# Optimization experiments

Hardware: AMD Instinct MI355X
Metric: run time of the kernel (lower is better)

## Reference

```python
import jax, jax.numpy as jnp
import numpy as np

B = 512
IMG = 32
NFF = 64
LAT_N = 256
LAT_C = 100
TOKEN_DIM = 3 + 2 * NFF  # 131
HEADS = 4
DEPTH = 2
MLP_HID = 4 * LAT_C
EPS = 1e-5


def _layernorm(x, g, b):
    mu = jnp.mean(x, axis=-1, keepdims=True)
    var = jnp.mean((x - mu) ** 2, axis=-1, keepdims=True)
    return (x - mu) * jax.lax.rsqrt(var + EPS) * g + b


def _mha(h, in_w, in_b, out_w, out_b):
    # torch nn.MultiheadAttention, batch_first, eval mode (no dropout)
    Bh, L, D = h.shape
    hd = D // HEADS
    qkv = h @ in_w.T + in_b  # [B, L, 3D]
    q, k, v = jnp.split(qkv, 3, axis=-1)
    def heads(t):
        return t.reshape(Bh, L, HEADS, hd).transpose(0, 2, 1, 3)  # [B,H,L,hd]
    q, k, v = heads(q), heads(k), heads(v)
    scores = jnp.einsum('bhqd,bhkd->bhqk', q, k) / jnp.sqrt(jnp.float32(hd))
    attn = jax.nn.softmax(scores, axis=-1)
    o = jnp.einsum('bhqk,bhkd->bhqd', attn, v)
    o = o.transpose(0, 2, 1, 3).reshape(Bh, L, D)
    return o @ out_w.T + out_b


def _forward(x, latents, latent_pos, fourier_matrix, proj_w, proj_b,
             q_w, q_b, k_w, k_b, v_w, v_b, o_w, o_b,
             ln1_g, ln1_b, attn_in_w, attn_in_b, attn_out_w, attn_out_b,
             ln2_g, ln2_b, mlp_w1, mlp_b1, mlp_w2, mlp_b2):
    Bx = x.shape[0]
    lat = (latents + latent_pos)[None].repeat(Bx, axis=0)  # [B, 256, 100]

    # per-pixel RGB tokens
    rgb = x.transpose(0, 2, 3, 1).reshape(Bx, -1, 3)  # [B, 1024, 3]

    # Fourier positional encoding
    yy, xx = jnp.meshgrid(jnp.arange(IMG, dtype=jnp.float32),
                          jnp.arange(IMG, dtype=jnp.float32), indexing='ij')
    coords = jnp.stack([xx / (IMG - 1), yy / (IMG - 1)], axis=-1).reshape(-1, 2)  # [1024, 2]
    proj = coords @ fourier_matrix  # [1024, NFF]
    pos = jnp.concatenate([jnp.cos(2 * jnp.pi * proj), jnp.sin(2 * jnp.pi * proj)], axis=-1)
    pos = jnp.broadcast_to(pos[None], (Bx, IMG * IMG, 2 * NFF))

    tokens = jnp.concatenate([rgb, pos], axis=-1)  # [B, 1024, 131]
    tokens = tokens @ proj_w.T + proj_b  # [B, 1024, 100]

    # K/V depend only on (fixed) tokens, identical across the 8 iterations
    k = tokens @ k_w.T + k_b
    v = tokens @ v_w.T + v_b

    scale = 1.0 / jnp.sqrt(jnp.float32(LAT_C))
    for _ in range(8):
        q = lat @ q_w.T + q_b  # [B, 256, 100]
        attn = jax.nn.softmax(jnp.einsum('bqc,bkc->bqk', q, k) * scale, axis=-1)
        lat = jnp.einsum('bqk,bkc->bqc', attn, v) @ o_w.T + o_b
        # latent transformer (depth=2, shared across the 8 iterations)
        for d in range(DEPTH):
            h = _layernorm(lat, ln1_g[d], ln1_b[d])
            lat = lat + _mha(h, attn_in_w[d], attn_in_b[d], attn_out_w[d], attn_out_b[d])
            h = _layernorm(lat, ln2_g[d], ln2_b[d])
            h = jax.nn.gelu(h @ mlp_w1[d].T + mlp_b1[d], approximate=False) @ mlp_w2[d].T + mlp_b2[d]
            lat = lat + h
    return lat.mean(axis=1)  # [B, 100]


def setup_inputs() -> dict:
    key = jax.random.key(0)
    ks = jax.random.split(key, 32)
    s = 0.02
    inp = {
        'x': jax.random.normal(ks[0], (B, 3, IMG, IMG), jnp.float32),
        'latents': jax.random.normal(ks[1], (LAT_N, LAT_C), jnp.float32),
        'latent_pos': jax.random.normal(ks[2], (LAT_N, LAT_C), jnp.float32),
        'fourier_matrix': jax.random.normal(ks[3], (2, NFF), jnp.float32),
        'proj_w': jax.random.normal(ks[4], (LAT_C, TOKEN_DIM), jnp.float32) * s,
        'proj_b': jnp.zeros((LAT_C,), jnp.float32),
        'q_w': jax.random.normal(ks[5], (LAT_C, LAT_C), jnp.float32) * s,
        'q_b': jnp.zeros((LAT_C,), jnp.float32),
        'k_w': jax.random.normal(ks[6], (LAT_C, LAT_C), jnp.float32) * s,
        'k_b': jnp.zeros((LAT_C,), jnp.float32),
        'v_w': jax.random.normal(ks[7], (LAT_C, LAT_C), jnp.float32) * s,
        'v_b': jnp.zeros((LAT_C,), jnp.float32),
        'o_w': jax.random.normal(ks[8], (LAT_C, LAT_C), jnp.float32) * s,
        'o_b': jnp.zeros((LAT_C,), jnp.float32),
        'ln1_g': jnp.ones((DEPTH, LAT_C), jnp.float32),
        'ln1_b': jnp.zeros((DEPTH, LAT_C), jnp.float32),
        'attn_in_w': jax.random.normal(ks[9], (DEPTH, 3 * LAT_C, LAT_C), jnp.float32) * s,
        'attn_in_b': jnp.zeros((DEPTH, 3 * LAT_C), jnp.float32),
        'attn_out_w': jax.random.normal(ks[10], (DEPTH, LAT_C, LAT_C), jnp.float32) * s,
        'attn_out_b': jnp.zeros((DEPTH, LAT_C), jnp.float32),
        'ln2_g': jnp.ones((DEPTH, LAT_C), jnp.float32),
        'ln2_b': jnp.zeros((DEPTH, LAT_C), jnp.float32),
        'mlp_w1': jax.random.normal(ks[11], (DEPTH, MLP_HID, LAT_C), jnp.float32) * s,
        'mlp_b1': jnp.zeros((DEPTH, MLP_HID), jnp.float32),
        'mlp_w2': jax.random.normal(ks[12], (DEPTH, LAT_C, MLP_HID), jnp.float32) * s,
        'mlp_b2': jnp.zeros((DEPTH, LAT_C), jnp.float32),
    }
    return inp


def reference(x, latents, latent_pos, fourier_matrix, proj_w, proj_b,
              q_w, q_b, k_w, k_b, v_w, v_b, o_w, o_b,
              ln1_g, ln1_b, attn_in_w, attn_in_b, attn_out_w, attn_out_b,
              ln2_g, ln2_b, mlp_w1, mlp_b1, mlp_w2, mlp_b2):
    return _forward(x, latents, latent_pos, fourier_matrix, proj_w, proj_b,
                    q_w, q_b, k_w, k_b, v_w, v_b, o_w, o_b,
                    ln1_g, ln1_b, attn_in_w, attn_in_b, attn_out_w, attn_out_b,
                    ln2_g, ln2_b, mlp_w1, mlp_b1, mlp_w2, mlp_b2)
```

## Files before the change

### kernel.cpp

```cpp
#include <hip/hip_runtime.h>
#include <cmath>

#define WS_AK 0
#define WS_AV 300
#define WS_U  600

#define UW_DK   0
#define UW_DV   106496
#define UW_QW   212992
#define UW_OW   227328
#define UW_W1   241664
#define UW_W2   344064
#define UW_AIW  444416
#define UW_AOW  542720
#define UW_WCNT 358400

typedef __attribute__((ext_vector_type(8))) short short8;
typedef __attribute__((ext_vector_type(4))) float f32x4;

#define MFMA(a, b, c) __builtin_amdgcn_mfma_f32_16x16x32_bf16((a), (b), (c), 0, 0, 0)

static __device__ __forceinline__ unsigned short f2bf(float f) {
  unsigned int u = __float_as_uint(f);
  u += 0x7FFF + ((u >> 16) & 1);
  return (unsigned short)(u >> 16);
}
static __device__ __forceinline__ float bf2f(unsigned short u) {
  return __uint_as_float(((unsigned int)u) << 16);
}
static __device__ __forceinline__ f32x4 zero4() { return (f32x4){0.f, 0.f, 0.f, 0.f}; }

__global__ void pre_amat_kernel(const float* __restrict__ proj_w,
                                const float* __restrict__ k_w,
                                const float* __restrict__ v_w,
                                float* __restrict__ ws) {
  int idx = blockIdx.x * blockDim.x + threadIdx.x;
  if (idx >= 600) return;
  int sel = idx / 300;
  int rem = idx % 300;
  int c = rem / 100, m = rem % 100;
  const float* w = sel ? v_w : k_w;
  float acc = 0.f;
  for (int n = 0; n < 100; ++n) acc += proj_w[n * 131 + c] * w[m * 100 + n];
  ws[(sel ? WS_AV : WS_AK) + c * 100 + m] = acc;
}

__global__ void pre_dmat_kernel(const float* __restrict__ fm,
                                const float* __restrict__ proj_w,
                                const float* __restrict__ proj_b,
                                const float* __restrict__ k_w,
                                const float* __restrict__ k_b,
                                const float* __restrict__ v_w,
                                const float* __restrict__ v_b,
                                unsigned short* __restrict__ uw) {
  __shared__ float pos[8][128];
  __shared__ float tc[8][100];
  int p0 = blockIdx.x * 8;
  int tid = threadIdx.x;
  for (int idx = tid; idx < 1024; idx += 256) {
    int pl = idx >> 7, f = idx & 127;
    int p = p0 + pl;
    float cx = (float)(p & 31) * (1.f / 31.f);
    float cy = (float)(p >> 5) * (1.f / 31.f);
    int fi = f & 63;
    float pr = cx * fm[fi] + cy * fm[64 + fi];
    float ang = 6.2831853071795864769f * pr;
    pos[pl][f] = (f < 64) ? cosf(ang) : sinf(ang);
  }
  __syncthreads();
  for (int idx = tid; idx < 800; idx += 256) {
    int pl = idx / 100, n = idx % 100;
    float acc = proj_b[n];
    const float* pw = proj_w + n * 131 + 3;
    for (int f = 0; f < 128; ++f) acc += pos[pl][f] * pw[f];
    tc[pl][n] = acc;
  }
  __syncthreads();
  for (int idx = tid; idx < 1600; idx += 256) {
    int sel = idx / 800;
    int rem = idx % 800;
    int pl = rem / 100, m = rem % 100;
    const float* w = sel ? v_w : k_w;
    float acc = sel ? v_b[m] : k_b[m];
    for (int n = 0; n < 100; ++n) acc += tc[pl][n] * w[m * 100 + n];
    if (sel) uw[UW_DV + m * 1024 + (p0 + pl)] = f2bf(acc);
    else     uw[UW_DK + (p0 + pl) * 104 + m] = f2bf(acc);
  }
  for (int idx = tid; idx < 32; idx += 256) {
    int pl = idx >> 2, mm = 100 + (idx & 3);
    uw[UW_DK + (p0 + pl) * 104 + mm] = 0;
  }
}

__global__ void pre_wfrag_kernel(const float* __restrict__ q_w,
                                 const float* __restrict__ o_w,
                                 const float* __restrict__ mlp_w1,
                                 const float* __restrict__ mlp_w2,
                                 const float* __restrict__ attn_in_w,
                                 const float* __restrict__ attn_out_w,
                                 unsigned short* __restrict__ uw) {
  int idx = blockIdx.x * 256 + threadIdx.x;
  if (idx >= UW_WCNT) return;
  float val = 0.f;
  if (idx < 14336) {
    int rem = idx;
    int kt = rem / 3584; rem %= 3584;
    int nt = rem / 512;  rem %= 512;
    int lane = rem >> 3, j = rem & 7;
    int k = kt * 32 + (lane >> 4) * 8 + j;
    int n = nt * 16 + (lane & 15);
    if (k < 100 && n < 100) val = q_w[n * 100 + k];
  } else if (idx < 28672) {
    int rem = idx - 14336;
    int kt = rem / 3584; rem %= 3584;
    int nt = rem / 512;  rem %= 512;
    int lane = rem >> 3, j = rem & 7;
    int k = kt * 32 + (lane >> 4) * 8 + j;
    int n = nt * 16 + (lane & 15);
    if (k < 100 && n < 100) val = o_w[n * 100 + k];
  } else if (idx < 131072) {
    int off = idx - 28672;
    int dd = off / 51200;
    int rem = off % 51200;
    int kt = rem / 12800; rem %= 12800;
    int nt = rem / 512;   rem %= 512;
    int lane = rem >> 3, j = rem & 7;
    int k = kt * 32 + (lane >> 4) * 8 + j;
    int n = nt * 16 + (lane & 15);
    if (k < 100) val = mlp_w1[dd * 40000 + n * 100 + k];
  } else if (idx < 231424) {
    int off = idx - 131072;
    int dd = off / 50176;
    int rem = off % 50176;
    int kt = rem / 3584; rem %= 3584;
    int nt = rem / 512;  rem %= 512;
    int lane = rem >> 3, j = rem & 7;
    int k = kt * 32 + (lane >> 4) * 8 + j;
    int n = nt * 16 + (lane & 15);
    if (k < 400 && n < 100) val = mlp_w2[dd * 40000 + n * 400 + k];
  } else if (idx < 329728) {
    int off = idx - 231424;
    int dw = off / 16384;
    int rem = off % 16384;
    int dd = dw / 3, wsel = dw % 3;
    int kt = rem / 4096; rem %= 4096;
    int nt = rem / 512;  rem %= 512;
    int lane = rem >> 3, j = rem & 7;
    int k = kt * 32 + (lane >> 4) * 8 + j;
    int np = nt * 16 + (lane & 15);
    int hh = np >> 5, dh = np & 31;
    if (k < 100 && dh < 25)
      val = attn_in_w[dd * 30000 + (wsel * 100 + hh * 25 + dh) * 100 + k];
  } else {
    int off = idx - 329728;
    int dd = off / 14336;
    int rem = off % 14336;
    int kt = rem / 3584; rem %= 3584;
    int nt = rem / 512;  rem %= 512;
    int lane = rem >> 3, j = rem & 7;
    int kp = kt * 32 + (lane >> 4) * 8 + j;
    int hh = kp >> 5, dh = kp & 31;
    int n = nt * 16 + (lane & 15);
    if (dh < 25 && n < 100)
      val = attn_out_w[dd * 10000 + n * 100 + hh * 25 + dh];
  }
  uw[UW_QW + idx] = f2bf(val);
}

__launch_bounds__(512, 1)
__global__ void perceiver_kernel(
    const float* __restrict__ x,
    const float* __restrict__ latents,
    const float* __restrict__ latent_pos,
    const float* __restrict__ q_b, const float* __restrict__ o_b,
    const float* __restrict__ ln1_g, const float* __restrict__ ln1_b,
    const float* __restrict__ attn_in_b, const float* __restrict__ attn_out_b,
    const float* __restrict__ ln2_g, const float* __restrict__ ln2_b,
    const float* __restrict__ mlp_b1, const float* __restrict__ mlp_b2,
    const float* __restrict__ ws,
    float* __restrict__ out) {
  __shared__ __align__(16) float s_pool[39240];
  float* s_sm = s_pool;
  float* reg0 = s_pool + 3400;
  unsigned short* s_M  = (unsigned short*)reg0;
  unsigned short* s_Hb = (unsigned short*)(reg0 + 17408);
  unsigned short* sK = s_Hb;
  unsigned short* sV = s_Hb + 8192;
  unsigned short* sP = s_Hb + 15360;
  unsigned short* s_Qh  = s_Hb;
  unsigned short* kfrag = s_Hb + 10240;
  unsigned short* vfrag = s_Hb + 18432;
  unsigned short* sPm   = s_Hb + 26624;
  float* s_x = reg0;

  const int tid  = threadIdx.x;
  const int b    = blockIdx.x;
  const int r    = tid >> 1;
  const int half = tid & 1;
  const int hc   = half * 50;
  const int lane = tid & 63;
  const int wv   = tid >> 6;
  const int li   = lane & 15;
  const int lg   = lane >> 4;
  const unsigned short* uw = (const unsigned short*)(ws + WS_U);

  for (int i = tid; i < 100; i += 512) { s_sm[i] = q_b[i]; s_sm[100 + i] = o_b[i]; }
  for (int i = tid; i < 200; i += 512) {
    s_sm[200 + i] = ln1_g[i]; s_sm[400 + i] = ln1_b[i];
    s_sm[600 + i] = ln2_g[i]; s_sm[800 + i] = ln2_b[i];
    s_sm[1600 + i] = attn_out_b[i]; s_sm[2600 + i] = mlp_b2[i];
  }
  for (int i = tid; i < 600; i += 512) s_sm[1000 + i] = attn_in_b[i];
  for (int i = tid; i < 800; i += 512) s_sm[1800 + i] = mlp_b1[i];
  for (int i = tid; i < 300; i += 512) { s_sm[2800 + i] = ws[WS_AK + i]; s_sm[3100 + i] = ws[WS_AV + i]; }

  float latv[50];
  #pragma unroll
  for (int i = 0; i < 50; ++i)
    latv[i] = latents[r * 100 + hc + i] + latent_pos[r * 100 + hc + i];

  const float* xb = x + (long)b * 3072;

  for (int it = 0; it < 8; ++it) {
    __syncthreads();
    #pragma unroll
    for (int i = 0; i < 50; ++i) s_M[r * 136 + hc + i] = f2bf(latv[i]);
    #pragma unroll
    for (int i = 0; i < 14; ++i) s_M[r * 136 + 100 + half * 14 + i] = 0;
    __syncthreads();

    {
      f32x4 qacc[2][7];
      #pragma unroll
      for (int a0 = 0; a0 < 2; ++a0)
        #pragma unroll
        for (int a1 = 0; a1 < 7; ++a1) qacc[a0][a1] = zero4();
      short8 aq[2][4];
      #pragma unroll
      for (int mt2 = 0; mt2 < 2; ++mt2)
        #pragma unroll
        for (int kt = 0; kt < 4; ++kt)
          aq[mt2][kt] = *(const short8*)(s_M + ((2 * wv + mt2) * 16 + li) * 136 + kt * 32 + lg * 8);
      #pragma unroll
      for (int nt = 0; nt < 7; ++nt)
        #pragma unroll
        for (int kt = 0; kt < 4; ++kt) {
          short8 bw = *(const short8*)(uw + UW_QW + ((kt * 7 + nt) * 64 + lane) * 8);
          #pragma unroll
          for (int mt2 = 0; mt2 < 2; ++mt2) qacc[mt2][nt] = MFMA(aq[mt2][kt], bw, qacc[mt2][nt]);
        }
      #pragma unroll
      for (int mt2 = 0; mt2 < 2; ++mt2)
        #pragma unroll
        for (int nt = 0; nt < 7; ++nt) {
          int col = nt * 16 + li;
          if (col < 100) {
            #pragma unroll
            for (int rg = 0; rg < 4; ++rg) {
              int row = (2 * wv + mt2) * 16 + lg * 4 + rg;
              s_M[row * 136 + col] = f2bf((qacc[mt2][nt][rg] + s_sm[col]) * 0.1f);
            }
          }
        }
    }

    f32x4 O[2][7];
    #pragma unroll
    for (int a0 = 0; a0 < 2; ++a0)
      #pragma unroll
      for (int a1 = 0; a1 < 7; ++a1) O[a0][a1] = zero4();
    short8 aq2[2][4];
    #pragma unroll
    for (int mt2 = 0; mt2 < 2; ++mt2)
      #pragma unroll
      for (int kt = 0; kt < 4; ++kt)
        aq2[mt2][kt] = *(const short8*)(s_M + ((2 * wv + mt2) * 16 + li) * 136 + kt * 32 + lg * 8);

    for (int t0 = 0; t0 < 1024; t0 += 64) {
      __syncthreads();
      for (int vi = tid; vi < 1024; vi += 512) {
        const int key = vi & 63, cg = vi >> 6;
        const int p = t0 + key;
        short8 w;
        if (cg < 13) {
          const float xr = xb[p], xg = xb[1024 + p], xv = xb[2048 + p];
          short8 dk = *(const short8*)(uw + UW_DK + p * 104 + cg * 8);
          #pragma unroll
          for (int e = 0; e < 8; ++e) {
            const int c = cg * 8 + e;
            float val = 0.f;
            if (c < 100)
              val = xr * s_sm[2800 + c] + xg * s_sm[2900 + c] + xv * s_sm[3000 + c]
                  + bf2f((unsigned short)w[0] * 0 + (unsigned short)dk[e]);
            w[e] = (short)f2bf(val);
          }
        } else {
          #pragma unroll
          for (int e = 0; e < 8; ++e) w[e] = 0;
        }
        *(short8*)(sK + vi * 8) = w;
      }
      for (int vi = tid; vi < 896; vi += 512) {
        const int ch = vi % 112, kg = vi / 112;
        const int pv0 = t0 + kg * 8;
        short8 w;
        if (ch < 100) {
          const float4 xr0 = *(const float4*)(xb + pv0);
          const float4 xr1 = *(const float4*)(xb + pv0 + 4);
          const float4 xg0 = *(const float4*)(xb + 1024 + pv0);
          const float4 xg1 = *(const float4*)(xb + 1024 + pv0 + 4);
          const float4 xv0 = *(const float4*)(xb + 2048 + pv0);
          const float4 xv1 = *(const float4*)(xb + 2048 + pv0 + 4);
          short8 dv = *(const short8*)(uw + UW_DV + ch * 1024 + pv0);
          const float a0 = s_sm[3100 + ch], a1 = s_sm[3200 + ch], a2 = s_sm[3300 + ch];
          const float xrv[8] = {xr0.x, xr0.y, xr0.z, xr0.w, xr1.x, xr1.y, xr1.z, xr1.w};
          const float xgv[8] = {xg0.x, xg0.y, xg0.z, xg0.w, xg1.x, xg1.y, xg1.z, xg1.w};
          const float xvv[8] = {xv0.x, xv0.y, xv0.z, xv0.w, xv1.x, xv1.y, xv1.z, xv1.w};
          #pragma unroll
          for (int e = 0; e < 8; ++e)
            w[e] = (short)f2bf(xrv[e] * a0 + xgv[e] * a1 + xvv[e] * a2
                               + bf2f((unsigned short)dv[e]));
        } else if (ch == 100) {
          #pragma unroll
          for (int e = 0; e < 8; ++e) w[e] = (short)0x3F80;
        } else {
          #pragma unroll
          for (int e = 0; e < 8; ++e) w[e] = 0;
        }
        *(short8*)(sV + vi * 8) = w;
      }
      __syncthreads();

      #pragma unroll
      for (int ntk = 0; ntk < 4; ++ntk) {
        short8 bk[4];
        #pragma unroll
        for (int kt = 0; kt < 4; ++kt)
          bk[kt] = *(const short8*)(sK + ((kt * 4 + lg) * 64 + ntk * 16 + li) * 8);
        #pragma unroll
        for (int mt2 = 0; mt2 < 2; ++mt2) {
          f32x4 sres = zero4();
          #pragma unroll
          for (int kt = 0; kt < 4; ++kt) sres = MFMA(aq2[mt2][kt], bk[kt], sres);
          #pragma unroll
          for (int rg = 0; rg < 4; ++rg) {
            int row = (2 * wv + mt2) * 16 + lg * 4 + rg;
            sP[row * 72 + ntk * 16 + li] = f2bf(__expf(sres[rg]));
          }
        }
      }
      short8 ap[2][2];
      #pragma unroll
      for (int mt2 = 0; mt2 < 2; ++mt2)
        #pragma unroll
        for (int kt2 = 0; kt2 < 2; ++kt2)
          ap[mt2][kt2] = *(const short8*)(sP + ((2 * wv + mt2) * 16 + li) * 72 + kt2 * 32 + lg * 8);
      #pragma unroll
      for (int nt = 0; nt < 7; ++nt) {
        short8 bv0 = *(const short8*)(sV + ((0 + lg) * 112 + nt * 16 + li) * 8);
        short8 bv1 = *(const short8*)(sV + ((4 + lg) * 112 + nt * 16 + li) * 8);
        #pragma unroll
        for (int mt2 = 0; mt2 < 2; ++mt2) {
          O[mt2][nt] = MFMA(ap[mt2][0], bv0, O[mt2][nt]);
          O[mt2][nt] = MFMA(ap[mt2][1], bv1, O[mt2][nt]);
        }
      }
    }

    {
      #pragma unroll
      for (int mt2 = 0; mt2 < 2; ++mt2) {
        float linv[4];
        #pragma unroll
        for (int rg = 0; rg < 4; ++rg) {
          float lv = __shfl(O[mt2][6][rg], (lane & 48) + 4);
          linv[rg] = 1.0f / lv;
        }
        #pragma unroll
        for (int nt = 0; nt < 7; ++nt) {
          int col = nt * 16 + li;
          if (col < 100) {
            #pragma unroll
            for (int rg = 0; rg < 4; ++rg) {
              int row = (2 * wv + mt2) * 16 + lg * 4 + rg;
              s_M[row * 136 + col] = f2bf(O[mt2][nt][rg] * linv[rg]);
            }
          }
        }
      }
    }

    {
      f32x4 lacc[2][7];
      #pragma unroll
      for (int a0 = 0; a0 < 2; ++a0)
        #pragma unroll
        for (int a1 = 0; a1 < 7; ++a1) lacc[a0][a1] = zero4();
      short8 ao[2][4];
      #pragma unroll
      for (int mt2 = 0; mt2 < 2; ++mt2)
        #pragma unroll
        for (int kt = 0; kt < 4; ++kt)
          ao[mt2][kt] = *(const short8*)(s_M + ((2 * wv + mt2) * 16 + li) * 136 + kt * 32 + lg * 8);
      #pragma unroll
      for (int nt = 0; nt < 7; ++nt)
        #pragma unroll
        for (int kt = 0; kt < 4; ++kt) {
          short8 bw = *(const short8*)(uw + UW_OW + ((kt * 7 + nt) * 64 + lane) * 8);
          #pragma unroll
          for (int mt2 = 0; mt2 < 2; ++mt2) lacc[mt2][nt] = MFMA(ao[mt2][kt], bw, lacc[mt2][nt]);
        }
      __syncthreads();
      #pragma unroll
      for (int mt2 = 0; mt2 < 2; ++mt2)
        #pragma unroll
        for (int nt = 0; nt < 7; ++nt) {
          int col = nt * 16 + li;
          if (col < 100) {
            #pragma unroll
            for (int rg = 0; rg < 4; ++rg) {
              int row = (2 * wv + mt2) * 16 + lg * 4 + rg;
              s_x[row * 104 + col] = lacc[mt2][nt][rg] + s_sm[100 + col];
            }
          }
        }
      __syncthreads();
      #pragma unroll
      for (int i = 0; i < 50; ++i) latv[i] = s_x[r * 104 + hc + i];
      __syncthreads();
    }

    for (int d = 0; d < 2; ++d) {
      float hv[50];
      {
        float s = 0.f, sq = 0.f;
        #pragma unroll
        for (int i = 0; i < 50; ++i) { s += latv[i]; sq += latv[i] * latv[i]; }
        s += __shfl_xor(s, 1); sq += __shfl_xor(sq, 1);
        float mu = s * 0.01f;
        float var = sq * 0.01f - mu * mu;
        float rs = rsqrtf(var + 1e-5f);
        #pragma unroll
        for (int i = 0; i < 50; ++i)
          hv[i] = (latv[i] - mu) * rs * s_sm[200 + d * 100 + hc + i] + s_sm[400 + d * 100 + hc + i];
      }

      #pragma unroll
      for (int i = 0; i < 50; ++i) s_M[r * 136 + hc + i] = f2bf(hv[i]);
      #pragma unroll
      for (int i = 0; i < 14; ++i) s_M[r * 136 + 100 + half * 14 + i] = 0;
      short8 ah[2][4];
      #pragma unroll
      for (int mt2 = 0; mt2 < 2; ++mt2)
        #pragma unroll
        for (int kt = 0; kt < 4; ++kt)
          ah[mt2][kt] = *(const short8*)(s_M + ((2 * wv + mt2) * 16 + li) * 136 + kt * 32 + lg * 8);

      for (int h = 0; h < 4; ++h) {
        __syncthreads();
        f32x4 cq[2][2], ck[2][2], cv[2][2];
        #pragma unroll
        for (int a0 = 0; a0 < 2; ++a0)
          #pragma unroll
          for (int a1 = 0; a1 < 2; ++a1) { cq[a0][a1] = zero4(); ck[a0][a1] = zero4(); cv[a0][a1] = zero4(); }
        #pragma unroll
        for (int ntd = 0; ntd < 2; ++ntd)
          #pragma unroll
          for (int kt = 0; kt < 4; ++kt) {
            const int bidx = ((kt * 8 + h * 2 + ntd) * 64 + lane) * 8;
            short8 bq  = *(const short8*)(uw + UW_AIW + (d * 3 + 0) * 16384 + bidx);
            short8 bkk = *(const short8*)(uw + UW_AIW + (d * 3 + 1) * 16384 + bidx);
            short8 bvv = *(const short8*)(uw + UW_AIW + (d * 3 + 2) * 16384 + bidx);
            #pragma unroll
            for (int mt2 = 0; mt2 < 2; ++mt2) {
              cq[mt2][ntd] = MFMA(ah[mt2][kt], bq,  cq[mt2][ntd]);
              ck[mt2][ntd] = MFMA(ah[mt2][kt], bkk, ck[mt2][ntd]);
              cv[mt2][ntd] = MFMA(ah[mt2][kt], bvv, cv[mt2][ntd]);
            }
          }
        #pragma unroll
        for (int mt2 = 0; mt2 < 2; ++mt2)
          #pragma unroll
          for (int ntd = 0; ntd < 2; ++ntd) {
            const int dh = ntd * 16 + li;
            const bool ok = dh < 25;
            const float qb2 = ok ? s_sm[1000 + d * 300 +       h * 25 + dh] : 0.f;
            const float kb2 = ok ? s_sm[1000 + d * 300 + 100 + h * 25 + dh] : 0.f;
            const float vb2 = ok ? s_sm[1000 + d * 300 + 200 + h * 25 + dh] : 0.f;
            #pragma unroll
            for (int rg = 0; rg < 4; ++rg) {
              const int rr = lg * 4 + rg;
              const int row = (2 * wv + mt2) * 16 + rr;
              s_Qh[row * 40 + dh] = ok ? f2bf((cq[mt2][ntd][rg] + qb2) * 0.2f) : 0;
              kfrag[((2 * wv + mt2) * 64 + (dh >> 3) * 16 + rr) * 8 + (dh & 7)] =
                  ok ? f2bf(ck[mt2][ntd][rg] + kb2) : 0;
              vfrag[((wv * 2 + ntd) * 64 + (mt2 * 2 + (rr >> 3)) * 16 + li) * 8 + (rr & 7)] =
                  ok ? f2bf(cv[mt2][ntd][rg] + vb2)
                     : (unsigned short)((dh == 25) ? 0x3F80 : 0);
            }
          }
        __syncthreads();
        short8 aqh[2];
        #pragma unroll
        for (int mt2 = 0; mt2 < 2; ++mt2)
          aqh[mt2] = *(const short8*)(s_Qh + ((2 * wv + mt2) * 16 + li) * 40 + lg * 8);
        f32x4 Oh[2][2];
        #pragma unroll
        for (int a0 = 0; a0 < 2; ++a0)
          #pragma unroll
          for (int a1 = 0; a1 < 2; ++a1) Oh[a0][a1] = zero4();
        for (int t = 0; t < 8; ++t) {
          short8 bk0 = *(const short8*)(kfrag + ((t * 2 + 0) * 64 + lane) * 8);
          short8 bk1 = *(const short8*)(kfrag + ((t * 2 + 1) * 64 + lane) * 8);
          f32x4 sres[2][2];
          #pragma unroll
          for (int mt2 = 0; mt2 < 2; ++mt2) {
            sres[mt2][0] = MFMA(aqh[mt2], bk0, zero4());
            sres[mt2][1] = MFMA(aqh[mt2], bk1, zero4());
          }
          #pragma unroll
          for (int mt2 = 0; mt2 < 2; ++mt2)
            #pragma unroll
            for (int ntk = 0; ntk < 2; ++ntk)
              #pragma unroll
              for (int rg = 0; rg < 4; ++rg) {
                const int row = (2 * wv + mt2) * 16 + lg * 4 + rg;
                sPm[row * 40 + ntk * 16 + li] = f2bf(__expf(sres[mt2][ntk][rg]));
              }
          short8 ap0 = *(const short8*)(sPm + ((2 * wv + 0) * 16 + li) * 40 + lg * 8);
          short8 ap1 = *(const short8*)(sPm + ((2 * wv + 1) * 16 + li) * 40 + lg * 8);
          short8 bv0 = *(const short8*)(vfrag + ((t * 2 + 0) * 64 + lane) * 8);
          short8 bv1 = *(const short8*)(vfrag + ((t * 2 + 1) * 64 + lane) * 8);
          Oh[0][0] = MFMA(ap0, bv0, Oh[0][0]);
          Oh[0][1] = MFMA(ap0, bv1, Oh[0][1]);
          Oh[1][0] = MFMA(ap1, bv0, Oh[1][0]);
          Oh[1][1] = MFMA(ap1, bv1, Oh[1][1]);
        }
        #pragma unroll
        for (int mt2 = 0; mt2 < 2; ++mt2)
          #pragma unroll
          for (int rg = 0; rg < 4; ++rg) {
            const float lv = __shfl(Oh[mt2][1][rg], (lane & 48) + 9);
            const float linv = 1.0f / lv;
            #pragma unroll
            for (int ntv = 0; ntv < 2; ++ntv) {
              const int dh = ntv * 16 + li;
              const int row = (2 * wv + mt2) * 16 + lg * 4 + rg;
              s_M[row * 136 + h * 32 + dh] =
                  (dh < 25) ? f2bf(Oh[mt2][ntv][rg] * linv) : 0;
            }
          }
      }
      __syncthreads();
      {
        short8 ao[2][4];
        #pragma unroll
        for (int mt2 = 0; mt2 < 2; ++mt2)
          #pragma unroll
          for (int kt = 0; kt < 4; ++kt)
            ao[mt2][kt] = *(const short8*)(s_M + ((2 * wv + mt2) * 16 + li) * 136 + kt * 32 + lg * 8);
        __syncthreads();
        f32x4 co[2][7];
        #pragma unroll
        for (int a0 = 0; a0 < 2; ++a0)
          #pragma unroll
          for (int a1 = 0; a1 < 7; ++a1) co[a0][a1] = zero4();
        #pragma unroll
        for (int nt = 0; nt < 7; ++nt)
          #pragma unroll
          for (int kt = 0; kt < 4; ++kt) {
            short8 bw = *(const short8*)(uw + UW_AOW + d * 14336 + ((kt * 7 + nt) * 64 + lane) * 8);
            #pragma unroll
            for (int mt2 = 0; mt2 < 2; ++mt2) co[mt2][nt] = MFMA(ao[mt2][kt], bw, co[mt2][nt]);
          }
        #pragma unroll
        for (int mt2 = 0; mt2 < 2; ++mt2)
          #pragma unroll
          for (int nt = 0; nt < 7; ++nt) {
            const int col = nt * 16 + li;
            if (col < 100) {
              #pragma unroll
              for (int rg = 0; rg < 4; ++rg) {
                const int row = (2 * wv + mt2) * 16 + lg * 4 + rg;
                s_x[row * 104 + col] = co[mt2][nt][rg] + s_sm[1600 + d * 100 + col];
              }
            }
          }
        #pragma unroll
        for (int i = 0; i < 50; ++i) latv[i] += s_x[r * 104 + hc + i];
      }

      {
        float s = 0.f, sq = 0.f;
        #pragma unroll
        for (int i = 0; i < 50; ++i) { s += latv[i]; sq += latv[i] * latv[i]; }
        s += __shfl_xor(s, 1); sq += __shfl_xor(sq, 1);
        float mu = s * 0.01f;
        float var = sq * 0.01f - mu * mu;
        float rs = rsqrtf(var + 1e-5f);
        #pragma unroll
        for (int i = 0; i < 50; ++i)
          hv[i] = (latv[i] - mu) * rs * s_sm[600 + d * 100 + hc + i] + s_sm[800 + d * 100 + hc + i];
      }

      __syncthreads();
      #pragma unroll
      for (int i = 0; i < 50; ++i) s_M[r * 136 + hc + i] = f2bf(hv[i]);
      #pragma unroll
      for (int i = 0; i < 14; ++i) s_M[r * 136 + 100 + half * 14 + i] = 0;
      __syncthreads();

      {
        const int w1off = UW_W1 + d * 51200;
        const int w2off = UW_W2 + d * 50176;
        f32x4 c2[2][7];
        #pragma unroll
        for (int a0 = 0; a0 < 2; ++a0)
          #pragma unroll
          for (int a1 = 0; a1 < 7; ++a1) c2[a0][a1] = zero4();
        short8 ahm[2][4];
        #pragma unroll
        for (int mt2 = 0; mt2 < 2; ++mt2)
          #pragma unroll
          for (int kt = 0; kt < 4; ++kt)
            ahm[mt2][kt] = *(const short8*)(s_M + ((2 * wv + mt2) * 16 + li) * 136 + kt * 32 + lg * 8);

        for (int chunk = 0; chunk < 3; ++chunk) {
          f32x4 c1[2][8];
          #pragma unroll
          for (int a0 = 0; a0 < 2; ++a0)
            #pragma unroll
            for (int a1 = 0; a1 < 8; ++a1) c1[a0][a1] = zero4();
          #pragma unroll
          for (int ntl = 0; ntl < 8; ++ntl)
            #pragma unroll
            for (int kt = 0; kt < 4; ++kt) {
              short8 bw = *(const short8*)(uw + w1off + ((kt * 25 + (chunk * 8 + ntl)) * 64 + lane) * 8);
              #pragma unroll
              for (int mt2 = 0; mt2 < 2; ++mt2) c1[mt2][ntl] = MFMA(ahm[mt2][kt], bw, c1[mt2][ntl]);
            }
          #pragma unroll
          for (int mt2 = 0; mt2 < 2; ++mt2)
            #pragma unroll
            for (int ntl = 0; ntl < 8; ++ntl) {
              int col = ntl * 16 + li;
              #pragma unroll
              for (int rg = 0; rg < 4; ++rg) {
                int row = (2 * wv + mt2) * 16 + lg * 4 + rg;
                float hval = c1[mt2][ntl][rg] + s_sm[1800 + d * 400 + chunk * 128 + col];
                float ge = 0.5f * hval * (1.0f + erff(hval * 0.70710678118654752f));
                s_Hb[row * 136 + col] = f2bf(ge);
              }
            }
          #pragma unroll
          for (int ktl = 0; ktl < 4; ++ktl) {
            short8 ahh[2];
            #pragma unroll
            for (int mt2 = 0; mt2 < 2; ++mt2)
              ahh[mt2] = *(const short8*)(s_Hb + ((2 * wv + mt2) * 16 + li) * 136 + ktl * 32 + lg * 8);
            #pragma unroll
            for (int nt = 0; nt < 7; ++nt) {
              short8 bw = *(const short8*)(uw + w2off + (((chunk * 4 + ktl) * 7 + nt) * 64 + lane) * 8);
              #pragma unroll
              for (int mt2 = 0; mt2 < 2; ++mt2) c2[mt2][nt] = MFMA(ahh[mt2], bw, c2[mt2][nt]);
            }
          }
        }
        {
          f32x4 c1a[2];
          c1a[0] = zero4(); c1a[1] = zero4();
          #pragma unroll
          for (int kt = 0; kt < 4; ++kt) {
            short8 bw = *(const short8*)(uw + w1off + ((kt * 25 + 24) * 64 + lane) * 8);
            #pragma unroll
            for (int mt2 = 0; mt2 < 2; ++mt2) c1a[mt2] = MFMA(ahm[mt2][kt], bw, c1a[mt2]);
          }
          #pragma unroll
          for (int mt2 = 0; mt2 < 2; ++mt2) {
            int col = li;
            #pragma unroll
            for (int rg = 0; rg < 4; ++rg) {
              int row = (2 * wv + mt2) * 16 + lg * 4 + rg;
              float hval = c1a[mt2][rg] + s_sm[1800 + d * 400 + 384 + col];
              float ge = 0.5f * hval * (1.0f + erff(hval * 0.70710678118654752f));
              s_Hb[row * 136 + col] = f2bf(ge);
            }
          }
          for (int i = lane; i < 32 * 112; i += 64) {
            int rr2 = i / 112, cc = 16 + i % 112;
            s_Hb[(32 * wv + rr2) * 136 + cc] = 0;
          }
          short8 ahh[2];
          #pragma unroll
          for (int mt2 = 0; mt2 < 2; ++mt2)
            ahh[mt2] = *(const short8*)(s_Hb + ((2 * wv + mt2) * 16 + li) * 136 + lg * 8);
          #pragma unroll
          for (int nt = 0; nt < 7; ++nt) {
            short8 bw = *(const short8*)(uw + w2off + ((12 * 7 + nt) * 64 + lane) * 8);
            #pragma unroll
            for (int mt2 = 0; mt2 < 2; ++mt2) c2[mt2][nt] = MFMA(ahh[mt2], bw, c2[mt2][nt]);
          }
        }
        __syncthreads();
        #pragma unroll
        for (int mt2 = 0; mt2 < 2; ++mt2)
          #pragma unroll
          for (int nt = 0; nt < 7; ++nt) {
            int col = nt * 16 + li;
            if (col < 100) {
              #pragma unroll
              for (int rg = 0; rg < 4; ++rg) {
                int row = (2 * wv + mt2) * 16 + lg * 4 + rg;
                s_x[row * 104 + col] = c2[mt2][nt][rg];
              }
            }
          }
        __syncthreads();
        #pragma unroll
        for (int i = 0; i < 50; ++i) latv[i] += s_x[r * 104 + hc + i] + s_sm[2600 + d * 100 + hc + i];
        __syncthreads();
      }
    }
  }

  for (int wd = 128; wd >= 1; wd >>= 1) {
    __syncthreads();
    if (r >= wd && r < 2 * wd) {
      #pragma unroll
      for (int i = 0; i < 50; ++i) reg0[(r - wd) * 100 + hc + i] = latv[i];
    }
    __syncthreads();
    if (r < wd) {
      #pragma unroll
      for (int i = 0; i < 50; ++i) latv[i] += reg0[r * 100 + hc + i];
    }
  }
  if (r == 0) {
    #pragma unroll
    for (int i = 0; i < 50; ++i) out[b * 100 + hc + i] = latv[i] * (1.0f / 256.0f);
  }
}

extern "C" void kernel_launch(void* const* d_in, const int* in_sizes, int n_in,
                              void* d_out, int out_size, void* d_ws, size_t ws_size,
                              hipStream_t stream) {
  (void)in_sizes; (void)n_in; (void)out_size; (void)ws_size;
  const float* x          = (const float*)d_in[0];
  const float* latents    = (const float*)d_in[1];
  const float* latent_pos = (const float*)d_in[2];
  const float* fm         = (const float*)d_in[3];
  const float* proj_w     = (const float*)d_in[4];
  const float* proj_b     = (const float*)d_in[5];
  const float* q_w        = (const float*)d_in[6];
  const float* q_b        = (const float*)d_in[7];
  const float* k_w        = (const float*)d_in[8];
  const float* k_b        = (const float*)d_in[9];
  const float* v_w        = (const float*)d_in[10];
  const float* v_b        = (const float*)d_in[11];
  const float* o_w        = (const float*)d_in[12];
  const float* o_b        = (const float*)d_in[13];
  const float* ln1_g      = (const float*)d_in[14];
  const float* ln1_b      = (const float*)d_in[15];
  const float* attn_in_w  = (const float*)d_in[16];
  const float* attn_in_b  = (const float*)d_in[17];
  const float* attn_out_w = (const float*)d_in[18];
  const float* attn_out_b = (const float*)d_in[19];
  const float* ln2_g      = (const float*)d_in[20];
  const float* ln2_b      = (const float*)d_in[21];
  const float* mlp_w1     = (const float*)d_in[22];
  const float* mlp_b1     = (const float*)d_in[23];
  const float* mlp_w2     = (const float*)d_in[24];
  const float* mlp_b2     = (const float*)d_in[25];
  float* ws   = (float*)d_ws;
  float* outp = (float*)d_out;
  unsigned short* uw = (unsigned short*)(ws + WS_U);

  pre_amat_kernel<<<3, 256, 0, stream>>>(proj_w, k_w, v_w, ws);
  pre_dmat_kernel<<<128, 256, 0, stream>>>(fm, proj_w, proj_b, k_w, k_b, v_w, v_b, uw);
  pre_wfrag_kernel<<<(UW_WCNT + 255) / 256, 256, 0, stream>>>(
      q_w, o_w, mlp_w1, mlp_w2, attn_in_w, attn_out_w, uw);
  perceiver_kernel<<<512, 512, 0, stream>>>(
      x, latents, latent_pos, q_b, o_b,
      ln1_g, ln1_b, attn_in_b, attn_out_b,
      ln2_g, ln2_b, mlp_b1, mlp_b2, ws, outp);
}
```

Baseline: 6.634 ms.

## Keep latent state in MFMA accumulator layout and shrink LDS for higher occupancy

Latent activations now stay in registers in the MFMA C-fragment layout instead of a per-thread row layout, so LayerNorm uses lane shuffles and the residual adds happen in registers. This removes the LDS round trips and several __syncthreads per stage. The LDS pool shrinks from about 157 KB to about 81 KB and launch bounds ask for more resident blocks per CU. The trade-offs are tighter register pressure and some biases now read from global memory rather than shared memory.

```diff
diff --git a/kernel.cpp b/kernel.cpp
--- a/kernel.cpp
+++ b/kernel.cpp
@@ -167,7 +167,7 @@
   uw[UW_QW + idx] = f2bf(val);
 }
 
-__launch_bounds__(512, 1)
+__launch_bounds__(512, 4)
 __global__ void perceiver_kernel(
     const float* __restrict__ x,
     const float* __restrict__ latents,
@@ -179,102 +179,133 @@
     const float* __restrict__ mlp_b1, const float* __restrict__ mlp_b2,
     const float* __restrict__ ws,
     float* __restrict__ out) {
-  __shared__ __align__(16) float s_pool[39240];
+  __shared__ __align__(16) float s_pool[20208];
   float* s_sm = s_pool;
-  float* reg0 = s_pool + 3400;
-  unsigned short* s_M  = (unsigned short*)reg0;
-  unsigned short* s_Hb = (unsigned short*)(reg0 + 17408);
-  unsigned short* sK = s_Hb;
-  unsigned short* sV = s_Hb + 8192;
-  unsigned short* sP = s_Hb + 15360;
-  unsigned short* s_Qh  = s_Hb;
-  unsigned short* kfrag = s_Hb + 10240;
-  unsigned short* vfrag = s_Hb + 18432;
-  unsigned short* sPm   = s_Hb + 26624;
-  float* s_x = reg0;
+  float* Rf   = s_pool + 2800;
+  unsigned short* R   = (unsigned short*)Rf;
+  unsigned short* s_M = R;
+  unsigned short* sK  = R;
+  unsigned short* sV  = R + 8192;
+  unsigned short* sP  = R + 15360;
+  unsigned short* sQh   = R;
+  unsigned short* kfrag = R + 9216;
+  unsigned short* vfrag = R + 17408;
+  unsigned short* sPm   = R + 25600;
 
   const int tid  = threadIdx.x;
   const int b    = blockIdx.x;
-  const int r    = tid >> 1;
-  const int half = tid & 1;
-  const int hc   = half * 50;
   const int lane = tid & 63;
   const int wv   = tid >> 6;
   const int li   = lane & 15;
   const int lg   = lane >> 4;
   const unsigned short* uw = (const unsigned short*)(ws + WS_U);
 
-  for (int i = tid; i < 100; i += 512) { s_sm[i] = q_b[i]; s_sm[100 + i] = o_b[i]; }
   for (int i = tid; i < 200; i += 512) {
-    s_sm[200 + i] = ln1_g[i]; s_sm[400 + i] = ln1_b[i];
-    s_sm[600 + i] = ln2_g[i]; s_sm[800 + i] = ln2_b[i];
-    s_sm[1600 + i] = attn_out_b[i]; s_sm[2600 + i] = mlp_b2[i];
-  }
-  for (int i = tid; i < 600; i += 512) s_sm[1000 + i] = attn_in_b[i];
-  for (int i = tid; i < 800; i += 512) s_sm[1800 + i] = mlp_b1[i];
-  for (int i = tid; i < 300; i += 512) { s_sm[2800 + i] = ws[WS_AK + i]; s_sm[3100 + i] = ws[WS_AV + i]; }
-
-  float latv[50];
+    s_sm[i] = ln1_g[i]; s_sm[200 + i] = ln1_b[i];
+    s_sm[400 + i] = ln2_g[i]; s_sm[600 + i] = ln2_b[i];
+  }
+  for (int i = tid; i < 600; i += 512) s_sm[800 + i] = attn_in_b[i];
+  for (int i = tid; i < 800; i += 512) s_sm[1400 + i] = mlp_b1[i];
+  for (int i = tid; i < 300; i += 512) { s_sm[2200 + i] = ws[WS_AK + i]; s_sm[2500 + i] = ws[WS_AV + i]; }
+
+  f32x4 latC[2][7];
   #pragma unroll
-  for (int i = 0; i < 50; ++i)
-    latv[i] = latents[r * 100 + hc + i] + latent_pos[r * 100 + hc + i];
+  for (int mt2 = 0; mt2 < 2; ++mt2)
+    #pragma unroll
+    for (int nt = 0; nt < 7; ++nt) {
+      const int col = nt * 16 + li;
+      #pragma unroll
+      for (int rg = 0; rg < 4; ++rg) {
+        const int row = (2 * wv + mt2) * 16 + lg * 4 + rg;
+        latC[mt2][nt][rg] = (col < 100)
+            ? latents[row * 100 + col] + latent_pos[row * 100 + col] : 0.f;
+      }
+    }
 
   const float* xb = x + (long)b * 3072;
 
+  auto ln_stage = [&](const float* gg, const float* bb) {
+    #pragma unroll
+    for (int mt2 = 0; mt2 < 2; ++mt2)
+      #pragma unroll
+      for (int rg = 0; rg < 4; ++rg) {
+        float s = 0.f, sq = 0.f;
+        #pragma unroll
+        for (int nt = 0; nt < 7; ++nt) {
+          const int col = nt * 16 + li;
+          if (col < 100) { const float v = latC[mt2][nt][rg]; s += v; sq += v * v; }
+        }
+        s += __shfl_xor(s, 1); sq += __shfl_xor(sq, 1);
+        s += __shfl_xor(s, 2); sq += __shfl_xor(sq, 2);
+        s += __shfl_xor(s, 4); sq += __shfl_xor(sq, 4);
+        s += __shfl_xor(s, 8); sq += __shfl_xor(sq, 8);
+        const float mu = s * 0.01f;
+        const float rs = rsqrtf(sq * 0.01f - mu * mu + 1e-5f);
+        const int row = (2 * wv + mt2) * 16 + lg * 4 + rg;
+        #pragma unroll
+        for (int nt = 0; nt < 7; ++nt) {
+          const int col = nt * 16 + li;
+          s_M[row * 132 + col] = (col < 100)
+              ? f2bf((latC[mt2][nt][rg] - mu) * rs * gg[col] + bb[col]) : 0;
+        }
+        s_M[row * 132 + 112 + li] = 0;
+      }
+  };
+
   for (int it = 0; it < 8; ++it) {
-    __syncthreads();
     #pragma unroll
-    for (int i = 0; i < 50; ++i) s_M[r * 136 + hc + i] = f2bf(latv[i]);
-    #pragma unroll
-    for (int i = 0; i < 14; ++i) s_M[r * 136 + 100 + half * 14 + i] = 0;
-    __syncthreads();
+    for (int mt2 = 0; mt2 < 2; ++mt2)
+      #pragma unroll
+      for (int rg = 0; rg < 4; ++rg) {
+        const int row = (2 * wv + mt2) * 16 + lg * 4 + rg;
+        #pragma unroll
+        for (int nt = 0; nt < 7; ++nt) {
+          const int col = nt * 16 + li;
+          s_M[row * 132 + col] = (col < 100) ? f2bf(latC[mt2][nt][rg]) : 0;
+        }
+        s_M[row * 132 + 112 + li] = 0;
+      }
 
     {
-      f32x4 qacc[2][7];
-      #pragma unroll
-      for (int a0 = 0; a0 < 2; ++a0)
-        #pragma unroll
-        for (int a1 = 0; a1 < 7; ++a1) qacc[a0][a1] = zero4();
       short8 aq[2][4];
       #pragma unroll
       for (int mt2 = 0; mt2 < 2; ++mt2)
         #pragma unroll
         for (int kt = 0; kt < 4; ++kt)
-          aq[mt2][kt] = *(const short8*)(s_M + ((2 * wv + mt2) * 16 + li) * 136 + kt * 32 + lg * 8);
-      #pragma unroll
-      for (int nt = 0; nt < 7; ++nt)
+          aq[mt2][kt] = *(const short8*)(s_M + ((2 * wv + mt2) * 16 + li) * 132 + kt * 32 + lg * 8);
+      #pragma unroll
+      for (int nt = 0; nt < 7; ++nt) {
+        f32x4 a0 = zero4(), a1 = zero4();
         #pragma unroll
         for (int kt = 0; kt < 4; ++kt) {
           short8 bw = *(const short8*)(uw + UW_QW + ((kt * 7 + nt) * 64 + lane) * 8);
-          #pragma unroll
-          for (int mt2 = 0; mt2 < 2; ++mt2) qacc[mt2][nt] = MFMA(aq[mt2][kt], bw, qacc[mt2][nt]);
-        }
-      #pragma unroll
-      for (int mt2 = 0; mt2 < 2; ++mt2)
-        #pragma unroll
-        for (int nt = 0; nt < 7; ++nt) {
-          int col = nt * 16 + li;
-          if (col < 100) {
-            #pragma unroll
-            for (int rg = 0; rg < 4; ++rg) {
-              int row = (2 * wv + mt2) * 16 + lg * 4 + rg;
-              s_M[row * 136 + col] = f2bf((qacc[mt2][nt][rg] + s_sm[col]) * 0.1f);
-            }
-          }
-        }
+          a0 = MFMA(aq[0][kt], bw, a0);
+          a1 = MFMA(aq[1][kt], bw, a1);
+        }
+        const int col = nt * 16 + li;
+        const float qb = (col < 100) ? q_b[col] : 0.f;
+        #pragma unroll
+        for (int rg = 0; rg < 4; ++rg) {
+          const int r0 = (2 * wv) * 16 + lg * 4 + rg;
+          const int r1 = (2 * wv + 1) * 16 + lg * 4 + rg;
+          s_M[r0 * 132 + col] = (col < 100) ? f2bf((a0[rg] + qb) * 0.1f) : 0;
+          s_M[r1 * 132 + col] = (col < 100) ? f2bf((a1[rg] + qb) * 0.1f) : 0;
+        }
+      }
     }
+
+    short8 aq2[2][4];
+    #pragma unroll
+    for (int mt2 = 0; mt2 < 2; ++mt2)
+      #pragma unroll
+      for (int kt = 0; kt < 4; ++kt)
+        aq2[mt2][kt] = *(const short8*)(s_M + ((2 * wv + mt2) * 16 + li) * 132 + kt * 32 + lg * 8);
 
     f32x4 O[2][7];
     #pragma unroll
     for (int a0 = 0; a0 < 2; ++a0)
       #pragma unroll
       for (int a1 = 0; a1 < 7; ++a1) O[a0][a1] = zero4();
-    short8 aq2[2][4];
-    #pragma unroll
-    for (int mt2 = 0; mt2 < 2; ++mt2)
-      #pragma unroll
-      for (int kt = 0; kt < 4; ++kt)
-        aq2[mt2][kt] = *(const short8*)(s_M + ((2 * wv + mt2) * 16 + li) * 136 + kt * 32 + lg * 8);
 
     for (int t0 = 0; t0 < 1024; t0 += 64) {
       __syncthreads();
@@ -290,8 +321,8 @@
             const int c = cg * 8 + e;
             float val = 0.f;
             if (c < 100)
-              val = xr * s_sm[2800 + c] + xg * s_sm[2900 + c] + xv * s_sm[3000 + c]
-                  + bf2f((unsigned short)w[0] * 0 + (unsigned short)dk[e]);
+              val = xr * s_sm[2200 + c] + xg * s_sm[2300 + c] + xv * s_sm[2400 + c]
+                  + bf2f((unsigned short)dk[e]);
             w[e] = (short)f2bf(val);
           }
         } else {
@@ -312,7 +343,7 @@
           const float4 xv0 = *(const float4*)(xb + 2048 + pv0);
           const float4 xv1 = *(const float4*)(xb + 2048 + pv0 + 4);
           short8 dv = *(const short8*)(uw + UW_DV + ch * 1024 + pv0);
-          const float a0 = s_sm[3100 + ch], a1 = s_sm[3200 + ch], a2 = s_sm[3300 + ch];
+          const float a0 = s_sm[2500 + ch], a1 = s_sm[2600 + ch], a2 = s_sm[2700 + ch];
           const float xrv[8] = {xr0.x, xr0.y, xr0.z, xr0.w, xr1.x, xr1.y, xr1.z, xr1.w};
           const float xgv[8] = {xg0.x, xg0.y, xg0.z, xg0.w, xg1.x, xg1.y, xg1.z, xg1.w};
           const float xvv[8] = {xv0.x, xv0.y, xv0.z, xv0.w, xv1.x, xv1.y, xv1.z, xv1.w};
@@ -333,20 +364,19 @@
 
       #pragma unroll
       for (int ntk = 0; ntk < 4; ++ntk) {
-        short8 bk[4];
-        #pragma unroll
-        for (int kt = 0; kt < 4; ++kt)
-          bk[kt] = *(const short8*)(sK + ((kt * 4 + lg) * 64 + ntk * 16 + li) * 8);
-        #pragma unroll
-        for (int mt2 = 0; mt2 < 2; ++mt2) {
-          f32x4 sres = zero4();
-          #pragma unroll
-          for (int kt = 0; kt < 4; ++kt) sres = MFMA(aq2[mt2][kt], bk[kt], sres);
-          #pragma unroll
-          for (int rg = 0; rg < 4; ++rg) {
-            int row = (2 * wv + mt2) * 16 + lg * 4 + rg;
-            sP[row * 72 + ntk * 16 + li] = f2bf(__expf(sres[rg]));
-          }
+        f32x4 s0 = zero4(), s1 = zero4();
+        #pragma unroll
+        for (int kt = 0; kt < 4; ++kt) {
+          short8 bk = *(const short8*)(sK + ((kt * 4 + lg) * 64 + ntk * 16 + li) * 8);
+          s0 = MFMA(aq2[0][kt], bk, s0);
+          s1 = MFMA(aq2[1][kt], bk, s1);
+        }
+        #pragma unroll
+        for (int rg = 0; rg < 4; ++rg) {
+          const int r0 = (2 * wv) * 16 + lg * 4 + rg;
+          const int r1 = (2 * wv + 1) * 16 + lg * 4 + rg;
+          sP[r0 * 76 + ntk * 16 + li] = f2bf(__expf(s0[rg]));
+          sP[r1 * 76 + ntk * 16 + li] = f2bf(__expf(s1[rg]));
         }
       }
       short8 ap[2][2];
@@ -354,7 +384,7 @@
       for (int mt2 = 0; mt2 < 2; ++mt2)
         #pragma unroll
         for (int kt2 = 0; kt2 < 2; ++kt2)
-          ap[mt2][kt2] = *(const short8*)(sP + ((2 * wv + mt2) * 16 + li) * 72 + kt2 * 32 + lg * 8);
+          ap[mt2][kt2] = *(const short8*)(sP + ((2 * wv + mt2) * 16 + li) * 76 + kt2 * 32 + lg * 8);
       #pragma unroll
       for (int nt = 0; nt < 7; ++nt) {
         short8 bv0 = *(const short8*)(sV + ((0 + lg) * 112 + nt * 16 + li) * 8);
@@ -366,378 +396,269 @@
         }
       }
     }
+    __syncthreads();
+
+    #pragma unroll
+    for (int mt2 = 0; mt2 < 2; ++mt2)
+      #pragma unroll
+      for (int rg = 0; rg < 4; ++rg) {
+        const float lv = __shfl(O[mt2][6][rg], (lane & 48) + 4);
+        const float linv = 1.0f / lv;
+        const int row = (2 * wv + mt2) * 16 + lg * 4 + rg;
+        #pragma unroll
+        for (int nt = 0; nt < 7; ++nt) {
+          const int col = nt * 16 + li;
+          s_M[row * 132 + col] = (col < 100) ? f2bf(O[mt2][nt][rg] * linv) : 0;
+        }
+        s_M[row * 132 + 112 + li] = 0;
+      }
 
     {
-      #pragma unroll
-      for (int mt2 = 0; mt2 < 2; ++mt2) {
-        float linv[4];
-        #pragma unroll
-        for (int rg = 0; rg < 4; ++rg) {
-          float lv = __shfl(O[mt2][6][rg], (lane & 48) + 4);
-          linv[rg] = 1.0f / lv;
-        }
-        #pragma unroll
-        for (int nt = 0; nt < 7; ++nt) {
-          int col = nt * 16 + li;
-          if (col < 100) {
-            #pragma unroll
-            for (int rg = 0; rg < 4; ++rg) {
-              int row = (2 * wv + mt2) * 16 + lg * 4 + rg;
-              s_M[row * 136 + col] = f2bf(O[mt2][nt][rg] * linv[rg]);
-            }
-          }
-        }
-      }
-    }
-
-    {
-      f32x4 lacc[2][7];
-      #pragma unroll
-      for (int a0 = 0; a0 < 2; ++a0)
-        #pragma unroll
-        for (int a1 = 0; a1 < 7; ++a1) lacc[a0][a1] = zero4();
       short8 ao[2][4];
       #pragma unroll
       for (int mt2 = 0; mt2 < 2; ++mt2)
         #pragma unroll
         for (int kt = 0; kt < 4; ++kt)
-          ao[mt2][kt] = *(const short8*)(s_M + ((2 * wv + mt2) * 16 + li) * 136 + kt * 32 + lg * 8);
-      #pragma unroll
-      for (int nt = 0; nt < 7; ++nt)
+          ao[mt2][kt] = *(const short8*)(s_M + ((2 * wv + mt2) * 16 + li) * 132 + kt * 32 + lg * 8);
+      #pragma unroll
+      for (int nt = 0; nt < 7; ++nt) {
+        f32x4 a0 = zero4(), a1 = zero4();
         #pragma unroll
         for (int kt = 0; kt < 4; ++kt) {
           short8 bw = *(const short8*)(uw + UW_OW + ((kt * 7 + nt) * 64 + lane) * 8);
-          #pragma unroll
-          for (int mt2 = 0; mt2 < 2; ++mt2) lacc[mt2][nt] = MFMA(ao[mt2][kt], bw, lacc[mt2][nt]);
-        }
-      __syncthreads();
+          a0 = MFMA(ao[0][kt], bw, a0);
+          a1 = MFMA(ao[1][kt], bw, a1);
+        }
+        const int col = nt * 16 + li;
+        const float ob = (col < 100) ? o_b[col] : 0.f;
+        #pragma unroll
+        for (int rg = 0; rg < 4; ++rg) {
+          latC[0][nt][rg] = (col < 100) ? a0[rg] + ob : 0.f;
+          latC[1][nt][rg] = (col < 100) ? a1[rg] + ob : 0.f;
+        }
+      }
+    }
+
+    for (int d = 0; d < 2; ++d) {
+      ln_stage(&s_sm[d * 100], &s_sm[200 + d * 100]);
+      short8 ah[2][4];
       #pragma unroll
       for (int mt2 = 0; mt2 < 2; ++mt2)
         #pragma unroll
-        for (int nt = 0; nt < 7; ++nt) {
-          int col = nt * 16 + li;
-          if (col < 100) {
-            #pragma unroll
-            for (int rg = 0; rg < 4; ++rg) {
-              int row = (2 * wv + mt2) * 16 + lg * 4 + rg;
-              s_x[row * 104 + col] = lacc[mt2][nt][rg] + s_sm[100 + col];
-            }
-          }
-        }
-      __syncthreads();
-      #pragma unroll
-      for (int i = 0; i < 50; ++i) latv[i] = s_x[r * 104 + hc + i];
-      __syncthreads();
-    }
-
-    for (int d = 0; d < 2; ++d) {
-      float hv[50];
-      {
-        float s = 0.f, sq = 0.f;
-        #pragma unroll
-        for (int i = 0; i < 50; ++i) { s += latv[i]; sq += latv[i] * latv[i]; }
-        s += __shfl_xor(s, 1); sq += __shfl_xor(sq, 1);
-        float mu = s * 0.01f;
-        float var = sq * 0.01f - mu * mu;
-        float rs = rsqrtf(var + 1e-5f);
-        #pragma unroll
-        for (int i = 0; i < 50; ++i)
-          hv[i] = (latv[i] - mu) * rs * s_sm[200 + d * 100 + hc + i] + s_sm[400 + d * 100 + hc + i];
-      }
-
-      #pragma unroll
-      for (int i = 0; i < 50; ++i) s_M[r * 136 + hc + i] = f2bf(hv[i]);
-      #pragma unroll
-      for (int i = 0; i < 14; ++i) s_M[r * 136 + 100 + half * 14 + i] = 0;
-      short8 ah[2][4];
-      #pragma unroll
-      for (int mt2 = 0; mt2 < 2; ++mt2)
-        #pragma unroll
         for (int kt = 0; kt < 4; ++kt)
-          ah[mt2][kt] = *(const short8*)(s_M + ((2 * wv + mt2) * 16 + li) * 136 + kt * 32 + lg * 8);
+          ah[mt2][kt] = *(const short8*)(s_M + ((2 * wv + mt2) * 16 + li) * 132 + kt * 32 + lg * 8);
+
+      f32x4 co[2][7];
+      #pragma unroll
+      for (int nt = 0; nt < 7; ++nt) {
+        const int col = nt * 16 + li;
+        const float ob = (col < 100) ? attn_out_b[d * 100 + col] : 0.f;
+        #pragma unroll
+        for (int rg = 0; rg < 4; ++rg) {
+          co[0][nt][rg] = (col < 100) ? latC[0][nt][rg] + ob : 0.f;
+          co[1][nt][rg] = (col < 100) ? latC[1][nt][rg] + ob : 0.f;
+        }
+      }
 
       for (int h = 0; h < 4; ++h) {
         __syncthreads();
-        f32x4 cq[2][2], ck[2][2], cv[2][2];
-        #pragma unroll
-        for (int a0 = 0; a0 < 2; ++a0)
-          #pragma unroll
-          for (int a1 = 0; a1 < 2; ++a1) { cq[a0][a1] = zero4(); ck[a0][a1] = zero4(); cv[a0][a1] = zero4(); }
-        #pragma unroll
-        for (int ntd = 0; ntd < 2; ++ntd)
+        #pragma unroll
+        for (int ntd = 0; ntd < 2; ++ntd) {
+          f32x4 cq0 = zero4(), cq1 = zero4(), ck0 = zero4(), ck1 = zero4(),
+                cv0 = zero4(), cv1 = zero4();
           #pragma unroll
           for (int kt = 0; kt < 4; ++kt) {
             const int bidx = ((kt * 8 + h * 2 + ntd) * 64 + lane) * 8;
             short8 bq  = *(const short8*)(uw + UW_AIW + (d * 3 + 0) * 16384 + bidx);
             short8 bkk = *(const short8*)(uw + UW_AIW + (d * 3 + 1) * 16384 + bidx);
             short8 bvv = *(const short8*)(uw + UW_AIW + (d * 3 + 2) * 16384 + bidx);
-            #pragma unroll
-            for (int mt2 = 0; mt2 < 2; ++mt2) {
-              cq[mt2][ntd] = MFMA(ah[mt2][kt], bq,  cq[mt2][ntd]);
-              ck[mt2][ntd] = MFMA(ah[mt2][kt], bkk, ck[mt2][ntd]);
-              cv[mt2][ntd] = MFMA(ah[mt2][kt], bvv, cv[mt2][ntd]);
-            }
+            cq0 = MFMA(ah[0][kt], bq,  cq0); cq1 = MFMA(ah[1][kt], bq,  cq1);
+            ck0 = MFMA(ah[0][kt], bkk, ck0); ck1 = MFMA(ah[1][kt], bkk, ck1);
+            cv0 = MFMA(ah[0][kt], bvv, cv0); cv1 = MFMA(ah[1][kt], bvv, cv1);
           }
-        #pragma unroll
-        for (int mt2 = 0; mt2 < 2; ++mt2)
-          #pragma unroll
-          for (int ntd = 0; ntd < 2; ++ntd) {
-            const int dh = ntd * 16 + li;
-            const bool ok = dh < 25;
-            const float qb2 = ok ? s_sm[1000 + d * 300 +       h * 25 + dh] : 0.f;
-            const float kb2 = ok ? s_sm[1000 + d * 300 + 100 + h * 25 + dh] : 0.f;
-            const float vb2 = ok ? s_sm[1000 + d * 300 + 200 + h * 25 + dh] : 0.f;
+          const int dh = ntd * 16 + li;
+          const bool ok = dh < 25;
+          const float qb2 = ok ? s_sm[800 + d * 300 +       h * 25 + dh] : 0.f;
+          const float kb2 = ok ? s_sm[800 + d * 300 + 100 + h * 25 + dh] : 0.f;
+          const float vb2 = ok ? s_sm[800 + d * 300 + 200 + h * 25 + dh] : 0.f;
+          #pragma unroll
+          for (int mt2 = 0; mt2 < 2; ++mt2)
             #pragma unroll
             for (int rg = 0; rg < 4; ++rg) {
               const int rr = lg * 4 + rg;
               const int row = (2 * wv + mt2) * 16 + rr;
-              s_Qh[row * 40 + dh] = ok ? f2bf((cq[mt2][ntd][rg] + qb2) * 0.2f) : 0;
+              const float q = mt2 ? cq1[rg] : cq0[rg];
+              const float k = mt2 ? ck1[rg] : ck0[rg];
+              const float v = mt2 ? cv1[rg] : cv0[rg];
+              sQh[row * 36 + dh] = ok ? f2bf((q + qb2) * 0.2f) : 0;
               kfrag[((2 * wv + mt2) * 64 + (dh >> 3) * 16 + rr) * 8 + (dh & 7)] =
-                  ok ? f2bf(ck[mt2][ntd][rg] + kb2) : 0;
+                  ok ? f2bf(k + kb2) : 0;
               vfrag[((wv * 2 + ntd) * 64 + (mt2 * 2 + (rr >> 3)) * 16 + li) * 8 + (rr & 7)] =
-                  ok ? f2bf(cv[mt2][ntd][rg] + vb2)
-                     : (unsigned short)((dh == 25) ? 0x3F80 : 0);
+                  ok ? f2bf(v + vb2) : (unsigned short)((dh == 25) ? 0x3F80 : 0);
             }
-          }
+        }
         __syncthreads();
-        short8 aqh[2];
-        #pragma unroll
-        for (int mt2 = 0; mt2 < 2; ++mt2)
-          aqh[mt2] = *(const short8*)(s_Qh + ((2 * wv + mt2) * 16 + li) * 40 + lg * 8);
-        f32x4 Oh[2][2];
-        #pragma unroll
-        for (int a0 = 0; a0 < 2; ++a0)
-          #pragma unroll
-          for (int a1 = 0; a1 < 2; ++a1) Oh[a0][a1] = zero4();
+
+        short8 aqh0 = *(const short8*)(sQh + ((2 * wv + 0) * 16 + li) * 36 + lg * 8);
+        short8 aqh1 = *(const short8*)(sQh + ((2 * wv + 1) * 16 + li) * 36 + lg * 8);
+        f32x4 Oh00 = zero4(), Oh01 = zero4(), Oh10 = zero4(), Oh11 = zero4();
         for (int t = 0; t < 8; ++t) {
           short8 bk0 = *(const short8*)(kfrag + ((t * 2 + 0) * 64 + lane) * 8);
           short8 bk1 = *(const short8*)(kfrag + ((t * 2 + 1) * 64 + lane) * 8);
-          f32x4 sres[2][2];
-          #pragma unroll
-          for (int mt2 = 0; mt2 < 2; ++mt2) {
-            sres[mt2][0] = MFMA(aqh[mt2], bk0, zero4());
-            sres[mt2][1] = MFMA(aqh[mt2], bk1, zero4());
+          f32x4 s00 = MFMA(aqh0, bk0, zero4());
+          f32x4 s01 = MFMA(aqh0, bk1, zero4());
+          f32x4 s10 = MFMA(aqh1, bk0, zero4());
+          f32x4 s11 = MFMA(aqh1, bk1, zero4());
+          #pragma unroll
+          for (int rg = 0; rg < 4; ++rg) {
+            const int r0 = (2 * wv) * 16 + lg * 4 + rg;
+            const int r1 = (2 * wv + 1) * 16 + lg * 4 + rg;
+            sPm[r0 * 36 + li]      = f2bf(__expf(s00[rg]));
+            sPm[r0 * 36 + 16 + li] = f2bf(__expf(s01[rg]));
+            sPm[r1 * 36 + li]      = f2bf(__expf(s10[rg]));
+            sPm[r1 * 36 + 16 + li] = f2bf(__expf(s11[rg]));
           }
-          #pragma unroll
-          for (int mt2 = 0; mt2 < 2; ++mt2)
-            #pragma unroll
-            for (int ntk = 0; ntk < 2; ++ntk)
-              #pragma unroll
-              for (int rg = 0; rg < 4; ++rg) {
-                const int row = (2 * wv + mt2) * 16 + lg * 4 + rg;
-                sPm[row * 40 + ntk * 16 + li] = f2bf(__expf(sres[mt2][ntk][rg]));
-              }
-          short8 ap0 = *(const short8*)(sPm + ((2 * wv + 0) * 16 + li) * 40 + lg * 8);
-          short8 ap1 = *(const short8*)(sPm + ((2 * wv + 1) * 16 + li) * 40 + lg * 8);
+          short8 ap0 = *(const short8*)(sPm + ((2 * wv + 0) * 16 + li) * 36 + lg * 8);
+          short8 ap1 = *(const short8*)(sPm + ((2 * wv + 1) * 16 + li) * 36 + lg * 8);
           short8 bv0 = *(const short8*)(vfrag + ((t * 2 + 0) * 64 + lane) * 8);
           short8 bv1 = *(const short8*)(vfrag + ((t * 2 + 1) * 64 + lane) * 8);
-          Oh[0][0] = MFMA(ap0, bv0, Oh[0][0]);
-          Oh[0][1] = MFMA(ap0, bv1, Oh[0][1]);
-          Oh[1][0] = MFMA(ap1, bv0, Oh[1][0]);
-          Oh[1][1] = MFMA(ap1, bv1, Oh[1][1]);
+          Oh00 = MFMA(ap0, bv0, Oh00); Oh01 = MFMA(ap0, bv1, Oh01);
+          Oh10 = MFMA(ap1, bv0, Oh10); Oh11 = MFMA(ap1, bv1, Oh11);
         }
         #pragma unroll
         for (int mt2 = 0; mt2 < 2; ++mt2)
           #pragma unroll
           for (int rg = 0; rg < 4; ++rg) {
-            const float lv = __shfl(Oh[mt2][1][rg], (lane & 48) + 9);
+            const f32x4& o0 = mt2 ? Oh10 : Oh00;
+            const f32x4& o1 = mt2 ? Oh11 : Oh01;
+            const float lv = __shfl(o1[rg], (lane & 48) + 9);
             const float linv = 1.0f / lv;
-            #pragma unroll
-            for (int ntv = 0; ntv < 2; ++ntv) {
-              const int dh = ntv * 16 + li;
-              const int row = (2 * wv + mt2) * 16 + lg * 4 + rg;
-              s_M[row * 136 + h * 32 + dh] =
-                  (dh < 25) ? f2bf(Oh[mt2][ntv][rg] * linv) : 0;
-            }
+            const int row = (2 * wv + mt2) * 16 + lg * 4 + rg;
+            sPm[row * 36 + li]      = (li < 25)      ? f2bf(o0[rg] * linv) : 0;
+            sPm[row * 36 + 16 + li] = (16 + li < 25) ? f2bf(o1[rg] * linv) : 0;
           }
+        short8 ao0 = *(const short8*)(sPm + ((2 * wv + 0) * 16 + li) * 36 + lg * 8);
+        short8 ao1 = *(const short8*)(sPm + ((2 * wv + 1) * 16 + li) * 36 + lg * 8);
+        #pragma unroll
+        for (int nt = 0; nt < 7; ++nt) {
+          short8 bw = *(const short8*)(uw + UW_AOW + d * 14336 + ((h * 7 + nt) * 64 + lane) * 8);
+          co[0][nt] = MFMA(ao0, bw, co[0][nt]);
+          co[1][nt] = MFMA(ao1, bw, co[1][nt]);
+        }
       }
       __syncthreads();
+
+      #pragma unroll
+      for (int mt2 = 0; mt2 < 2; ++mt2)
+        #pragma unroll
+        for (int nt = 0; nt < 7; ++nt) latC[mt2][nt] = co[mt2][nt];
+
+      ln_stage(&s_sm[400 + d * 100], &s_sm[600 + d * 100]);
+      short8 ahm[2][4];
+      #pragma unroll
+      for (int mt2 = 0; mt2 < 2; ++mt2)
+        #pragma unroll
+        for (int kt = 0; kt < 4; ++kt)
+          ahm[mt2][kt] = *(const short8*)(s_M + ((2 * wv + mt2) * 16 + li) * 132 + kt * 32 + lg * 8);
+
+      f32x4 c2[2][7];
+      #pragma unroll
+      for (int nt = 0; nt < 7; ++nt) {
+        const int col = nt * 16 + li;
+        const float b2 = (col < 100) ? mlp_b2[d * 100 + col] : 0.f;
+        #pragma unroll
+        for (int rg = 0; rg < 4; ++rg) {
+          c2[0][nt][rg] = (col < 100) ? latC[0][nt][rg] + b2 : 0.f;
+          c2[1][nt][rg] = (col < 100) ? latC[1][nt][rg] + b2 : 0.f;
+        }
+      }
+
+      const int w1off = UW_W1 + d * 51200;
+      const int w2off = UW_W2 + d * 50176;
+      for (int chunk = 0; chunk < 3; ++chunk) {
+        #pragma unroll
+        for (int ntl = 0; ntl < 8; ++ntl) {
+          f32x4 a0 = zero4(), a1 = zero4();
+          #pragma unroll
+          for (int kt = 0; kt < 4; ++kt) {
+            short8 bw = *(const short8*)(uw + w1off + ((kt * 25 + (chunk * 8 + ntl)) * 64 + lane) * 8);
+            a0 = MFMA(ahm[0][kt], bw, a0);
+            a1 = MFMA(ahm[1][kt], bw, a1);
+          }
+          const int col = ntl * 16 + li;
+          const float bias = s_sm[1400 + d * 400 + chunk * 128 + col];
+          #pragma unroll
+          for (int rg = 0; rg < 4; ++rg) {
+            const int r0 = (2 * wv) * 16 + lg * 4 + rg;
+            const int r1 = (2 * wv + 1) * 16 + lg * 4 + rg;
+            float h0 = a0[rg] + bias, h1 = a1[rg] + bias;
+            s_M[r0 * 132 + col] = f2bf(0.5f * h0 * (1.0f + erff(h0 * 0.70710678118654752f)));
+            s_M[r1 * 132 + col] = f2bf(0.5f * h1 * (1.0f + erff(h1 * 0.70710678118654752f)));
+          }
+        }
+        #pragma unroll
+        for (int ktl = 0; ktl < 4; ++ktl) {
+          short8 ahh0 = *(const short8*)(s_M + ((2 * wv + 0) * 16 + li) * 132 + ktl * 32 + lg * 8);
+          short8 ahh1 = *(const short8*)(s_M + ((2 * wv + 1) * 16 + li) * 132 + ktl * 32 + lg * 8);
+          #pragma unroll
+          for (int nt = 0; nt < 7; ++nt) {
+            short8 bw = *(const short8*)(uw + w2off + (((chunk * 4 + ktl) * 7 + nt) * 64 + lane) * 8);
+            c2[0][nt] = MFMA(ahh0, bw, c2[0][nt]);
+            c2[1][nt] = MFMA(ahh1, bw, c2[1][nt]);
+          }
+        }
+      }
       {
-        short8 ao[2][4];
-        #pragma unroll
-        for (int mt2 = 0; mt2 < 2; ++mt2)
-          #pragma unroll
-          for (int kt = 0; kt < 4; ++kt)
-            ao[mt2][kt] = *(const short8*)(s_M + ((2 * wv + mt2) * 16 + li) * 136 + kt * 32 + lg * 8);
-        __syncthreads();
-        f32x4 co[2][7];
-        #pragma unroll
-        for (int a0 = 0; a0 < 2; ++a0)
-          #pragma unroll
-          for (int a1 = 0; a1 < 7; ++a1) co[a0][a1] = zero4();
-        #pragma unroll
-        for (int nt = 0; nt < 7; ++nt)
-          #pragma unroll
-          for (int kt = 0; kt < 4; ++kt) {
-            short8 bw = *(const short8*)(uw + UW_AOW + d * 14336 + ((kt * 7 + nt) * 64 + lane) * 8);
-            #pragma unroll
-            for (int mt2 = 0; mt2 < 2; ++mt2) co[mt2][nt] = MFMA(ao[mt2][kt], bw, co[mt2][nt]);
-          }
-        #pragma unroll
-        for (int mt2 = 0; mt2 < 2; ++mt2)
-          #pragma unroll
-          for (int nt = 0; nt < 7; ++nt) {
-            const int col = nt * 16 + li;
-            if (col < 100) {
-              #pragma unroll
-              for (int rg = 0; rg < 4; ++rg) {
-                const int row = (2 * wv + mt2) * 16 + lg * 4 + rg;
-                s_x[row * 104 + col] = co[mt2][nt][rg] + s_sm[1600 + d * 100 + col];
-              }
-            }
-          }
-        #pragma unroll
-        for (int i = 0; i < 50; ++i) latv[i] += s_x[r * 104 + hc + i];
-      }
-
-      {
-        float s = 0.f, sq = 0.f;
-        #pragma unroll
-        for (int i = 0; i < 50; ++i) { s += latv[i]; sq += latv[i] * latv[i]; }
-        s += __shfl_xor(s, 1); sq += __shfl_xor(sq, 1);
-        float mu = s * 0.01f;
-        float var = sq * 0.01f - mu * mu;
-        float rs = rsqrtf(var + 1e-5f);
-        #pragma unroll
-        for (int i = 0; i < 50; ++i)
-          hv[i] = (latv[i] - mu) * rs * s_sm[600 + d * 100 + hc + i] + s_sm[800 + d * 100 + hc + i];
-      }
-
-      __syncthreads();
-      #pragma unroll
-      for (int i = 0; i < 50; ++i) s_M[r * 136 + hc + i] = f2bf(hv[i]);
-      #pragma unroll
-      for (int i = 0; i < 14; ++i) s_M[r * 136 + 100 + half * 14 + i] = 0;
-      __syncthreads();
-
-      {
-        const int w1off = UW_W1 + d * 51200;
-        const int w2off = UW_W2 + d * 50176;
-        f32x4 c2[2][7];
-        #pragma unroll
-        for (int a0 = 0; a0 < 2; ++a0)
-          #pragma unroll
-          for (int a1 = 0; a1 < 7; ++a1) c2[a0][a1] = zero4();
-        short8 ahm[2][4];
-        #pragma unroll
-        for (int mt2 = 0; mt2 < 2; ++mt2)
-          #pragma unroll
-          for (int kt = 0; kt < 4; ++kt)
-            ahm[mt2][kt] = *(const short8*)(s_M + ((2 * wv + mt2) * 16 + li) * 136 + kt * 32 + lg * 8);
-
-        for (int chunk = 0; chunk < 3; ++chunk) {
-          f32x4 c1[2][8];
-          #pragma unroll
-          for (int a0 = 0; a0 < 2; ++a0)
-            #pragma unroll
-            for (int a1 = 0; a1 < 8; ++a1) c1[a0][a1] = zero4();
-          #pragma unroll
-          for (int ntl = 0; ntl < 8; ++ntl)
-            #pragma unroll
-            for (int kt = 0; kt < 4; ++kt) {
-              short8 bw = *(const short8*)(uw + w1off + ((kt * 25 + (chunk * 8 + ntl)) * 64 + lane) * 8);
-              #pragma unroll
-              for (int mt2 = 0; mt2 < 2; ++mt2) c1[mt2][ntl] = MFMA(ahm[mt2][kt], bw, c1[mt2][ntl]);
-            }
-          #pragma unroll
-          for (int mt2 = 0; mt2 < 2; ++mt2)
-            #pragma unroll
-            for (int ntl = 0; ntl < 8; ++ntl) {
-              int col = ntl * 16 + li;
-              #pragma unroll
-              for (int rg = 0; rg < 4; ++rg) {
-                int row = (2 * wv + mt2) * 16 + lg * 4 + rg;
-                float hval = c1[mt2][ntl][rg] + s_sm[1800 + d * 400 + chunk * 128 + col];
-                float ge = 0.5f * hval * (1.0f + erff(hval * 0.70710678118654752f));
-                s_Hb[row * 136 + col] = f2bf(ge);
-              }
-            }
-          #pragma unroll
-          for (int ktl = 0; ktl < 4; ++ktl) {
-            short8 ahh[2];
-            #pragma unroll
-            for (int mt2 = 0; mt2 < 2; ++mt2)
-              ahh[mt2] = *(const short8*)(s_Hb + ((2 * wv + mt2) * 16 + li) * 136 + ktl * 32 + lg * 8);
-            #pragma unroll
-            for (int nt = 0; nt < 7; ++nt) {
-              short8 bw = *(const short8*)(uw + w2off + (((chunk * 4 + ktl) * 7 + nt) * 64 + lane) * 8);
-              #pragma unroll
-              for (int mt2 = 0; mt2 < 2; ++mt2) c2[mt2][nt] = MFMA(ahh[mt2], bw, c2[mt2][nt]);
-            }
-          }
-        }
-        {
-          f32x4 c1a[2];
-          c1a[0] = zero4(); c1a[1] = zero4();
-          #pragma unroll
-          for (int kt = 0; kt < 4; ++kt) {
-            short8 bw = *(const short8*)(uw + w1off + ((kt * 25 + 24) * 64 + lane) * 8);
-            #pragma unroll
-            for (int mt2 = 0; mt2 < 2; ++mt2) c1a[mt2] = MFMA(ahm[mt2][kt], bw, c1a[mt2]);
-          }
-          #pragma unroll
-          for (int mt2 = 0; mt2 < 2; ++mt2) {
-            int col = li;
-            #pragma unroll
-            for (int rg = 0; rg < 4; ++rg) {
-              int row = (2 * wv + mt2) * 16 + lg * 4 + rg;
-              float hval = c1a[mt2][rg] + s_sm[1800 + d * 400 + 384 + col];
-              float ge = 0.5f * hval * (1.0f + erff(hval * 0.70710678118654752f));
-              s_Hb[row * 136 + col] = f2bf(ge);
-            }
-          }
-          for (int i = lane; i < 32 * 112; i += 64) {
-            int rr2 = i / 112, cc = 16 + i % 112;
-            s_Hb[(32 * wv + rr2) * 136 + cc] = 0;
-          }
-          short8 ahh[2];
-          #pragma unroll
-          for (int mt2 = 0; mt2 < 2; ++mt2)
-            ahh[mt2] = *(const short8*)(s_Hb + ((2 * wv + mt2) * 16 + li) * 136 + lg * 8);
-          #pragma unroll
-          for (int nt = 0; nt < 7; ++nt) {
-            short8 bw = *(const short8*)(uw + w2off + ((12 * 7 + nt) * 64 + lane) * 8);
-            #pragma unroll
-            for (int mt2 = 0; mt2 < 2; ++mt2) c2[mt2][nt] = MFMA(ahh[mt2], bw, c2[mt2][nt]);
-          }
-        }
-        __syncthreads();
-        #pragma unroll
-        for (int mt2 = 0; mt2 < 2; ++mt2)
-          #pragma unroll
-          for (int nt = 0; nt < 7; ++nt) {
-            int col = nt * 16 + li;
-            if (col < 100) {
-              #pragma unroll
-              for (int rg = 0; rg < 4; ++rg) {
-                int row = (2 * wv + mt2) * 16 + lg * 4 + rg;
-                s_x[row * 104 + col] = c2[mt2][nt][rg];
-              }
-            }
-          }
-        __syncthreads();
-        #pragma unroll
-        for (int i = 0; i < 50; ++i) latv[i] += s_x[r * 104 + hc + i] + s_sm[2600 + d * 100 + hc + i];
-        __syncthreads();
-      }
+        f32x4 a0 = zero4(), a1 = zero4();
+        #pragma unroll
+        for (int kt = 0; kt < 4; ++kt) {
+          short8 bw = *(const short8*)(uw + w1off + ((kt * 25 + 24) * 64 + lane) * 8);
+          a0 = MFMA(ahm[0][kt], bw, a0);
+          a1 = MFMA(ahm[1][kt], bw, a1);
+        }
+        const float bias = s_sm[1400 + d * 400 + 384 + li];
+        #pragma unroll
+        for (int rg = 0; rg < 4; ++rg) {
+          const int r0 = (2 * wv) * 16 + lg * 4 + rg;
+          const int r1 = (2 * wv + 1) * 16 + lg * 4 + rg;
+          float h0 = a0[rg] + bias, h1 = a1[rg] + bias;
+          s_M[r0 * 132 + li] = f2bf(0.5f * h0 * (1.0f + erff(h0 * 0.70710678118654752f)));
+          s_M[r1 * 132 + li] = f2bf(0.5f * h1 * (1.0f + erff(h1 * 0.70710678118654752f)));
+          s_M[r0 * 132 + 16 + li] = 0;
+          s_M[r1 * 132 + 16 + li] = 0;
+        }
+        short8 ahh0 = *(const short8*)(s_M + ((2 * wv + 0) * 16 + li) * 132 + lg * 8);
+        short8 ahh1 = *(const short8*)(s_M + ((2 * wv + 1) * 16 + li) * 132 + lg * 8);
+        #pragma unroll
+        for (int nt = 0; nt < 7; ++nt) {
+          short8 bw = *(const short8*)(uw + w2off + ((12 * 7 + nt) * 64 + lane) * 8);
+          c2[0][nt] = MFMA(ahh0, bw, c2[0][nt]);
+          c2[1][nt] = MFMA(ahh1, bw, c2[1][nt]);
+        }
+      }
+      #pragma unroll
+      for (int mt2 = 0; mt2 < 2; ++mt2)
+        #pragma unroll
+        for (int nt = 0; nt < 7; ++nt) latC[mt2][nt] = c2[mt2][nt];
     }
   }
 
-  for (int wd = 128; wd >= 1; wd >>= 1) {
-    __syncthreads();
-    if (r >= wd && r < 2 * wd) {
-      #pragma unroll
-      for (int i = 0; i < 50; ++i) reg0[(r - wd) * 100 + hc + i] = latv[i];
-    }
-    __syncthreads();
-    if (r < wd) {
-      #pragma unroll
-      for (int i = 0; i < 50; ++i) latv[i] += reg0[r * 100 + hc + i];
-    }
-  }
-  if (r == 0) {
+  __syncthreads();
+  #pragma unroll
+  for (int nt = 0; nt < 7; ++nt) {
+    float v = 0.f;
     #pragma unroll
-    for (int i = 0; i < 50; ++i) out[b * 100 + hc + i] = latv[i] * (1.0f / 256.0f);
+    for (int rg = 0; rg < 4; ++rg) v += latC[0][nt][rg] + latC[1][nt][rg];
+    v += __shfl_xor(v, 16);
+    v += __shfl_xor(v, 32);
+    if (lg == 0) Rf[wv * 112 + nt * 16 + li] = v;
+  }
+  __syncthreads();
+  if (tid < 100) {
+    float s = 0.f;
+    #pragma unroll
+    for (int w = 0; w < 8; ++w) s += Rf[w * 112 + tid];
+    out[b * 100 + tid] = s * (1.0f / 256.0f);
   }
 }
 
```

Measured after the change: 5.538 ms. -16.5%, faster.
